# Performance work log

Hardware: AMD Instinct MI355X
Metric: run time of the kernel (lower is better)

## Reference

```python
import jax, jax.numpy as jnp
import numpy as np

N_EMBD = 1024
D_FF = 4096
N_EXPERTS = 8
TOP_K = 2


def setup_inputs() -> dict:
    key = jax.random.key(0)
    k1, k2, k3, k4 = jax.random.split(key, 4)
    x = jax.random.normal(k1, (1, 2048, N_EMBD), dtype=jnp.float32)
    mask = jnp.ones((2048, N_EXPERTS), dtype=jnp.float32)
    Wr = jax.random.normal(k2, (N_EMBD, N_EXPERTS), dtype=jnp.float32) * 0.02
    W1 = jax.random.normal(k3, (N_EXPERTS, N_EMBD, D_FF), dtype=jnp.float32) * 0.02
    W2 = jax.random.normal(k4, (N_EXPERTS, D_FF, N_EMBD), dtype=jnp.float32) * 0.02
    return {"x": x, "mask": mask, "Wr": Wr, "W1": W1, "W2": W2}


def reference(x, mask, Wr, W1, W2):
    T = x.shape[0] * x.shape[1]
    xs = x.reshape(T, N_EMBD)                      # [T, d]
    router_logits = (xs @ Wr) * mask               # [T, E], masked as in MaskedMoE
    all_probs = jax.nn.softmax(router_logits, axis=-1)  # softmax_topk order
    weights, selected = jax.lax.top_k(all_probs, TOP_K)  # [T, K]
    # combine[t, e] = sum of routing weights where token t selected expert e
    combine = jnp.zeros((T, N_EXPERTS), dtype=xs.dtype)
    combine = combine.at[jnp.arange(T)[:, None], selected].add(weights)
    results = jnp.zeros_like(xs)
    for e in range(N_EXPERTS):  # fixed small expert count
        h = jax.nn.gelu(xs @ W1[e])                # [T, d_ff]
        out = h @ W2[e]                            # [T, d]
        results = results + combine[:, e:e + 1] * out
    return results.reshape(x.shape)
```

## Files before the change

### kernel.cpp

```cpp
#include <hip/hip_runtime.h>
#include <hip/hip_bf16.h>


#define T_TOK 2048
#define D_EMB 1024
#define DFF   4096
#define NE    8

typedef _Float16 f16x8 __attribute__((ext_vector_type(8)));
typedef _Float16 f16x4 __attribute__((ext_vector_type(4)));
typedef float    f32x4 __attribute__((ext_vector_type(4)));

__device__ __forceinline__ float gelu_tanh(float x) {
    const float c = 0.7978845608028654f;
    float z = c * (x + 0.044715f * x * x * x);
    float u = __expf(2.0f * z);
    float th = (u - 1.0f) / (u + 1.0f);
    return 0.5f * x * (1.0f + th);
}

__device__ __forceinline__ void gll(const void* g, void* l) {
    __builtin_amdgcn_global_load_lds((__attribute__((address_space(1))) void*)g,
                                     (__attribute__((address_space(3))) void*)l,
                                     16, 0, 0);
}

__global__ void k_zero(int* counts) {
    if (threadIdx.x < NE) counts[threadIdx.x] = 0;
}

__global__ __launch_bounds__(256) void k_cvt_x(const float4* __restrict__ x4,
                                               _Float16* __restrict__ xh) {
    int i = blockIdx.x * 256 + threadIdx.x;
    float4 v = x4[i];
    f16x4 o;
    o[0] = (_Float16)v.x; o[1] = (_Float16)v.y;
    o[2] = (_Float16)v.z; o[3] = (_Float16)v.w;
    *(f16x4*)(xh + (size_t)i * 4) = o;
}

__global__ __launch_bounds__(256) void k_transpose(
    const float* __restrict__ src, _Float16* __restrict__ dst,
    int src_ld, int dst_ld) {
    __shared__ float tile[64][65];
    int e = blockIdx.z;
    const float* S = src + (size_t)e * 4194304;
    _Float16* D = dst + (size_t)e * 4194304;
    int t = threadIdx.x;
    int kb = blockIdx.y * 64;
    int nb = blockIdx.x * 64;
#pragma unroll
    for (int i = 0; i < 4; i++) {
        int r = (t >> 4) + i * 16;
        int c = (t & 15) * 4;
        float4 v = *(const float4*)(S + (size_t)(kb + r) * src_ld + nb + c);
        tile[r][c + 0] = v.x; tile[r][c + 1] = v.y;
        tile[r][c + 2] = v.z; tile[r][c + 3] = v.w;
    }
    __syncthreads();
#pragma unroll
    for (int j = 0; j < 2; j++) {
        int idx = j * 256 + t;
        int n = idx >> 3, kc = idx & 7;
        f16x8 o;
#pragma unroll
        for (int u = 0; u < 8; u++) o[u] = (_Float16)tile[kc * 8 + u][n];
        *(f16x8*)(D + (size_t)(nb + n) * dst_ld + kb + kc * 8) = o;
    }
}

__global__ __launch_bounds__(256) void k_router(
    const float* __restrict__ x, const float* __restrict__ mask,
    const float* __restrict__ Wr,
    int* __restrict__ counts, int* __restrict__ elist,
    int* __restrict__ tok_e, int* __restrict__ tok_p, float* __restrict__ tok_w) {
    int wave = threadIdx.x >> 6;
    int lane = threadIdx.x & 63;
    int t = blockIdx.x * 4 + wave;
    if (t >= T_TOK) return;

    float acc[NE];
#pragma unroll
    for (int e = 0; e < NE; e++) acc[e] = 0.f;
    const float* xr = x + (size_t)t * D_EMB;
    for (int c = 0; c < D_EMB / 64; c++) {
        int i = c * 64 + lane;
        float xv = xr[i];
        const float* wr = Wr + (size_t)i * NE;
#pragma unroll
        for (int e = 0; e < NE; e++) acc[e] += xv * wr[e];
    }
#pragma unroll
    for (int e = 0; e < NE; e++) {
#pragma unroll
        for (int off = 32; off > 0; off >>= 1)
            acc[e] += __shfl_xor(acc[e], off);
    }
    if (lane == 0) {
        float p[NE];
        float mx = -1e30f;
#pragma unroll
        for (int e = 0; e < NE; e++) {
            p[e] = acc[e] * mask[t * NE + e];
            mx = fmaxf(mx, p[e]);
        }
        float s = 0.f;
#pragma unroll
        for (int e = 0; e < NE; e++) { p[e] = expf(p[e] - mx); s += p[e]; }
#pragma unroll
        for (int e = 0; e < NE; e++) p[e] /= s;
        int e0 = 0; float b0 = p[0];
#pragma unroll
        for (int e = 1; e < NE; e++) if (p[e] > b0) { b0 = p[e]; e0 = e; }
        int e1 = -1; float b1 = -1.f;
#pragma unroll
        for (int e = 0; e < NE; e++) if (e != e0 && p[e] > b1) { b1 = p[e]; e1 = e; }

        int pos0 = atomicAdd(&counts[e0], 1);
        elist[e0 * T_TOK + pos0] = t;
        tok_e[t * 2 + 0] = e0; tok_p[t * 2 + 0] = pos0; tok_w[t * 2 + 0] = b0;
        int pos1 = atomicAdd(&counts[e1], 1);
        elist[e1 * T_TOK + pos1] = t;
        tok_e[t * 2 + 1] = e1; tok_p[t * 2 + 1] = pos1; tok_w[t * 2 + 1] = b1;
    }
}

__global__ void k_prefix(const int* __restrict__ counts, int* __restrict__ base) {
    if (threadIdx.x == 0) {
        int s = 0;
        for (int e = 0; e < NE; e++) { base[e] = s; s += counts[e]; }
        base[NE] = s;
    }
}

__global__ __launch_bounds__(256) void k_gemm1(
    const _Float16* __restrict__ xh, const _Float16* __restrict__ BT,
    const int* __restrict__ counts, const int* __restrict__ base,
    const int* __restrict__ elist, _Float16* __restrict__ H) {
    int e = blockIdx.z;
    int cnt = counts[e];
    int p0 = blockIdx.y * 128;
    if (p0 >= cnt) return;
    int n0 = blockIdx.x * 128;
    const _Float16* B = BT + (size_t)e * 4194304;

    __shared__ _Float16 As[128 * 32];
    __shared__ _Float16 Bs[128 * 32];
    __shared__ int ttok[128];

    int tid = threadIdx.x;
    if (tid < 128) ttok[tid] = elist[e * T_TOK + min(p0 + tid, cnt - 1)];
    __syncthreads();

    int w = tid >> 6, lane = tid & 63;
    int c0 = tid, c1 = tid + 256;
    const _Float16* pA0 = xh + (size_t)ttok[c0 >> 2] * D_EMB + (c0 & 3) * 8;
    const _Float16* pA1 = xh + (size_t)ttok[c1 >> 2] * D_EMB + (c1 & 3) * 8;
    const _Float16* pB0 = B + (size_t)(n0 + (c0 >> 2)) * 1024 + (c0 & 3) * 8;
    const _Float16* pB1 = B + (size_t)(n0 + (c1 >> 2)) * 1024 + (c1 & 3) * 8;
    _Float16* ldsA0 = As + (w * 64) * 8;
    _Float16* ldsA1 = As + (256 + w * 64) * 8;
    _Float16* ldsB0 = Bs + (w * 64) * 8;
    _Float16* ldsB1 = Bs + (256 + w * 64) * 8;

    int wm = w >> 1, wn = w & 1;
    int lhi = lane >> 4, llo = lane & 15;
    const _Float16* arp = As + ((wm * 64 + llo) * 32 + lhi * 8);
    const _Float16* brp = Bs + ((wn * 64 + llo) * 32 + lhi * 8);

    f32x4 acc[4][4] = {};
    for (int k0 = 0; k0 < D_EMB; k0 += 32) {
        __syncthreads();
        gll(pA0, ldsA0); gll(pA1, ldsA1);
        gll(pB0, ldsB0); gll(pB1, ldsB1);
        pA0 += 32; pA1 += 32; pB0 += 32; pB1 += 32;
        __syncthreads();
        f16x8 a[4], b[4];
#pragma unroll
        for (int i = 0; i < 4; i++) {
            a[i] = *(const f16x8*)(arp + i * 512);
            b[i] = *(const f16x8*)(brp + i * 512);
        }
#pragma unroll
        for (int mt = 0; mt < 4; mt++)
#pragma unroll
            for (int nt = 0; nt < 4; nt++)
                acc[mt][nt] = __builtin_amdgcn_mfma_f32_16x16x32_f16(a[mt], b[nt], acc[mt][nt], 0, 0, 0);
    }

    int rowbase = base[e];
#pragma unroll
    for (int mt = 0; mt < 4; mt++) {
#pragma unroll
        for (int i = 0; i < 4; i++) {
            int p = p0 + wm * 64 + mt * 16 + lhi * 4 + i;
            if (p < cnt) {
                size_t rowoff = (size_t)(rowbase + p) * DFF + n0 + wn * 64 + llo;
#pragma unroll
                for (int nt = 0; nt < 4; nt++)
                    H[rowoff + nt * 16] = (_Float16)gelu_tanh(acc[mt][nt][i]);
            }
        }
    }
}

__global__ __launch_bounds__(256) void k_gemm2(
    const _Float16* __restrict__ H, const _Float16* __restrict__ BT,
    const int* __restrict__ counts, const int* __restrict__ base,
    float* __restrict__ O, int kh) {
    int e = blockIdx.z;
    int cnt = counts[e];
    int p0 = blockIdx.y * 128;
    if (p0 >= cnt) return;
    int n0 = blockIdx.x * 128;
    const _Float16* B = BT + (size_t)e * 4194304;
    int rowbase = base[e];

    __shared__ _Float16 As[128 * 32];
    __shared__ _Float16 Bs[128 * 32];

    int tid = threadIdx.x;
    int w = tid >> 6, lane = tid & 63;
    int c0 = tid, c1 = tid + 256;
    int r0 = rowbase + min(p0 + (c0 >> 2), cnt - 1);
    int r1 = rowbase + min(p0 + (c1 >> 2), cnt - 1);
    const _Float16* pA0 = H + (size_t)r0 * DFF + kh + (c0 & 3) * 8;
    const _Float16* pA1 = H + (size_t)r1 * DFF + kh + (c1 & 3) * 8;
    const _Float16* pB0 = B + (size_t)(n0 + (c0 >> 2)) * 4096 + kh + (c0 & 3) * 8;
    const _Float16* pB1 = B + (size_t)(n0 + (c1 >> 2)) * 4096 + kh + (c1 & 3) * 8;
    _Float16* ldsA0 = As + (w * 64) * 8;
    _Float16* ldsA1 = As + (256 + w * 64) * 8;
    _Float16* ldsB0 = Bs + (w * 64) * 8;
    _Float16* ldsB1 = Bs + (256 + w * 64) * 8;

    int wm = w >> 1, wn = w & 1;
    int lhi = lane >> 4, llo = lane & 15;
    const _Float16* arp = As + ((wm * 64 + llo) * 32 + lhi * 8);
    const _Float16* brp = Bs + ((wn * 64 + llo) * 32 + lhi * 8);

    f32x4 acc[4][4] = {};
    for (int k0 = 0; k0 < 2048; k0 += 32) {
        __syncthreads();
        gll(pA0, ldsA0); gll(pA1, ldsA1);
        gll(pB0, ldsB0); gll(pB1, ldsB1);
        pA0 += 32; pA1 += 32; pB0 += 32; pB1 += 32;
        __syncthreads();
        f16x8 a[4], b[4];
#pragma unroll
        for (int i = 0; i < 4; i++) {
            a[i] = *(const f16x8*)(arp + i * 512);
            b[i] = *(const f16x8*)(brp + i * 512);
        }
#pragma unroll
        for (int mt = 0; mt < 4; mt++)
#pragma unroll
            for (int nt = 0; nt < 4; nt++)
                acc[mt][nt] = __builtin_amdgcn_mfma_f32_16x16x32_f16(a[mt], b[nt], acc[mt][nt], 0, 0, 0);
    }

#pragma unroll
    for (int mt = 0; mt < 4; mt++) {
#pragma unroll
        for (int i = 0; i < 4; i++) {
            int p = p0 + wm * 64 + mt * 16 + lhi * 4 + i;
            if (p < cnt) {
                size_t o = (size_t)(rowbase + p) * D_EMB + n0 + wn * 64 + llo;
#pragma unroll
                for (int nt = 0; nt < 4; nt++)
                    O[o + nt * 16] = acc[mt][nt][i];
            }
        }
    }
}

__global__ __launch_bounds__(256) void k_final(
    const float* __restrict__ O0, const float* __restrict__ O1,
    const int* __restrict__ base,
    const int* __restrict__ tok_e, const int* __restrict__ tok_p,
    const float* __restrict__ tok_w, float* __restrict__ out) {
    int t = blockIdx.x;
    int r0 = base[tok_e[t * 2 + 0]] + tok_p[t * 2 + 0];
    int r1 = base[tok_e[t * 2 + 1]] + tok_p[t * 2 + 1];
    float w0 = tok_w[t * 2 + 0], w1 = tok_w[t * 2 + 1];
    int i = threadIdx.x * 4;
    float4 a0 = *(const float4*)(O0 + (size_t)r0 * D_EMB + i);
    float4 b0 = *(const float4*)(O1 + (size_t)r0 * D_EMB + i);
    float4 a1 = *(const float4*)(O0 + (size_t)r1 * D_EMB + i);
    float4 b1 = *(const float4*)(O1 + (size_t)r1 * D_EMB + i);
    float4 o;
    o.x = w0 * (a0.x + b0.x) + w1 * (a1.x + b1.x);
    o.y = w0 * (a0.y + b0.y) + w1 * (a1.y + b1.y);
    o.z = w0 * (a0.z + b0.z) + w1 * (a1.z + b1.z);
    o.w = w0 * (a0.w + b0.w) + w1 * (a1.w + b1.w);
    *(float4*)(out + (size_t)t * D_EMB + i) = o;
}

extern "C" void kernel_launch(void* const* d_in, const int* in_sizes, int n_in,
                              void* d_out, int out_size, void* d_ws, size_t ws_size,
                              hipStream_t stream) {
    const float* x    = (const float*)d_in[0];
    const float* mask = (const float*)d_in[1];
    const float* Wr   = (const float*)d_in[2];
    const float* W1   = (const float*)d_in[3];
    const float* W2   = (const float*)d_in[4];
    float* out = (float*)d_out;

    char* ws = (char*)d_ws;
    const size_t MB = 1024 * 1024;
    int*      counts = (int*)(ws + 0);
    int*      base   = (int*)(ws + 256);
    int*      elist  = (int*)(ws + 1024);
    int*      tok_e  = (int*)(ws + 1024 + 65536);
    int*      tok_p  = (int*)(ws + 1024 + 65536 + 16384);
    float*    tok_w  = (float*)(ws + 1024 + 65536 + 32768);
    _Float16* xh     = (_Float16*)(ws + 1 * MB);
    _Float16* W1T    = (_Float16*)(ws + 8 * MB);
    _Float16* W2T    = (_Float16*)(ws + 72 * MB);
    _Float16* H      = (_Float16*)(ws + 136 * MB);
    float*    O0     = (float*)(ws + 168 * MB);
    float*    O1     = (float*)(ws + 184 * MB);

    k_zero<<<1, 64, 0, stream>>>(counts);
    k_router<<<T_TOK / 4, 256, 0, stream>>>(x, mask, Wr, counts, elist, tok_e, tok_p, tok_w);
    k_prefix<<<1, 64, 0, stream>>>(counts, base);
    k_cvt_x<<<T_TOK * D_EMB / 4 / 256, 256, 0, stream>>>((const float4*)x, xh);
    k_transpose<<<dim3(64, 16, NE), 256, 0, stream>>>(W1, W1T, DFF, 1024);
    k_transpose<<<dim3(16, 64, NE), 256, 0, stream>>>(W2, W2T, D_EMB, 4096);

    k_gemm1<<<dim3(32, 16, NE), 256, 0, stream>>>(xh, W1T, counts, base, elist, H);
    k_gemm2<<<dim3(8, 16, NE), 256, 0, stream>>>(H, W2T, counts, base, O0, 0);
    k_gemm2<<<dim3(8, 16, NE), 256, 0, stream>>>(H, W2T, counts, base, O1, 2048);
    k_final<<<T_TOK, 256, 0, stream>>>(O0, O1, base, tok_e, tok_p, tok_w, out);
}
```

Measured before the change: 543.3 us.

## Fuse prep kernels, widen GEMM K-tile with swizzled LDS, split-K by four

```diff
diff --git a/kernel.cpp b/kernel.cpp
--- a/kernel.cpp
+++ b/kernel.cpp
@@ -8,15 +8,13 @@
 #define NE    8
 
 typedef _Float16 f16x8 __attribute__((ext_vector_type(8)));
-typedef _Float16 f16x4 __attribute__((ext_vector_type(4)));
 typedef float    f32x4 __attribute__((ext_vector_type(4)));
 
 __device__ __forceinline__ float gelu_tanh(float x) {
     const float c = 0.7978845608028654f;
     float z = c * (x + 0.044715f * x * x * x);
     float u = __expf(2.0f * z);
-    float th = (u - 1.0f) / (u + 1.0f);
-    return 0.5f * x * (1.0f + th);
+    return 0.5f * x * (1.0f + (u - 1.0f) / (u + 1.0f));
 }
 
 __device__ __forceinline__ void gll(const void* g, void* l) {
@@ -29,26 +27,79 @@
     if (threadIdx.x < NE) counts[threadIdx.x] = 0;
 }
 
-__global__ __launch_bounds__(256) void k_cvt_x(const float4* __restrict__ x4,
-                                               _Float16* __restrict__ xh) {
-    int i = blockIdx.x * 256 + threadIdx.x;
-    float4 v = x4[i];
-    f16x4 o;
-    o[0] = (_Float16)v.x; o[1] = (_Float16)v.y;
-    o[2] = (_Float16)v.z; o[3] = (_Float16)v.w;
-    *(f16x4*)(xh + (size_t)i * 4) = o;
+__global__ __launch_bounds__(256) void k_router(
+    const float* __restrict__ x, const float* __restrict__ mask,
+    const float* __restrict__ Wr, _Float16* __restrict__ xh,
+    int* __restrict__ counts, int* __restrict__ elist,
+    int* __restrict__ tok_e, int* __restrict__ tok_p, float* __restrict__ tok_w) {
+    int wave = threadIdx.x >> 6;
+    int lane = threadIdx.x & 63;
+    int t = blockIdx.x * 4 + wave;
+    if (t >= T_TOK) return;
+
+    float acc[NE];
+#pragma unroll
+    for (int e = 0; e < NE; e++) acc[e] = 0.f;
+    const float* xr = x + (size_t)t * D_EMB;
+    for (int c = 0; c < D_EMB / 64; c++) {
+        int i = c * 64 + lane;
+        float xv = xr[i];
+        xh[(size_t)t * D_EMB + i] = (_Float16)xv;
+        const float* wr = Wr + (size_t)i * NE;
+#pragma unroll
+        for (int e = 0; e < NE; e++) acc[e] += xv * wr[e];
+    }
+#pragma unroll
+    for (int e = 0; e < NE; e++) {
+#pragma unroll
+        for (int off = 32; off > 0; off >>= 1)
+            acc[e] += __shfl_xor(acc[e], off);
+    }
+    if (lane == 0) {
+        float p[NE];
+        float mx = -1e30f;
+#pragma unroll
+        for (int e = 0; e < NE; e++) {
+            p[e] = acc[e] * mask[t * NE + e];
+            mx = fmaxf(mx, p[e]);
+        }
+        float s = 0.f;
+#pragma unroll
+        for (int e = 0; e < NE; e++) { p[e] = expf(p[e] - mx); s += p[e]; }
+#pragma unroll
+        for (int e = 0; e < NE; e++) p[e] /= s;
+        int e0 = 0; float b0 = p[0];
+#pragma unroll
+        for (int e = 1; e < NE; e++) if (p[e] > b0) { b0 = p[e]; e0 = e; }
+        int e1 = -1; float b1 = -1.f;
+#pragma unroll
+        for (int e = 0; e < NE; e++) if (e != e0 && p[e] > b1) { b1 = p[e]; e1 = e; }
+
+        int pos0 = atomicAdd(&counts[e0], 1);
+        elist[e0 * T_TOK + pos0] = t;
+        tok_e[t * 2 + 0] = e0; tok_p[t * 2 + 0] = pos0; tok_w[t * 2 + 0] = b0;
+        int pos1 = atomicAdd(&counts[e1], 1);
+        elist[e1 * T_TOK + pos1] = t;
+        tok_e[t * 2 + 1] = e1; tok_p[t * 2 + 1] = pos1; tok_w[t * 2 + 1] = b1;
+    }
 }
 
 __global__ __launch_bounds__(256) void k_transpose(
-    const float* __restrict__ src, _Float16* __restrict__ dst,
-    int src_ld, int dst_ld) {
+    const float* __restrict__ W1, const float* __restrict__ W2,
+    _Float16* __restrict__ W1T, _Float16* __restrict__ W2T) {
     __shared__ float tile[64][65];
-    int e = blockIdx.z;
-    const float* S = src + (size_t)e * 4194304;
-    _Float16* D = dst + (size_t)e * 4194304;
+    int bz = blockIdx.z;
+    int e = bz & 7;
+    bool isW2 = bz >= 8;
+    const float* S = (isW2 ? W2 : W1) + (size_t)e * 4194304;
+    _Float16* D = (isW2 ? W2T : W1T) + (size_t)e * 4194304;
+    int src_ld = isW2 ? 1024 : 4096;
+    int dst_ld = isW2 ? 4096 : 1024;
+    int bx = blockIdx.x;
+    int nb, kb;
+    if (isW2) { nb = (bx & 15) * 64; kb = (bx >> 4) * 64; }
+    else      { nb = (bx & 63) * 64; kb = (bx >> 6) * 64; }
     int t = threadIdx.x;
-    int kb = blockIdx.y * 64;
-    int nb = blockIdx.x * 64;
 #pragma unroll
     for (int i = 0; i < 4; i++) {
         int r = (t >> 4) + i * 16;
@@ -69,83 +120,22 @@
     }
 }
 
-__global__ __launch_bounds__(256) void k_router(
-    const float* __restrict__ x, const float* __restrict__ mask,
-    const float* __restrict__ Wr,
-    int* __restrict__ counts, int* __restrict__ elist,
-    int* __restrict__ tok_e, int* __restrict__ tok_p, float* __restrict__ tok_w) {
-    int wave = threadIdx.x >> 6;
-    int lane = threadIdx.x & 63;
-    int t = blockIdx.x * 4 + wave;
-    if (t >= T_TOK) return;
-
-    float acc[NE];
-#pragma unroll
-    for (int e = 0; e < NE; e++) acc[e] = 0.f;
-    const float* xr = x + (size_t)t * D_EMB;
-    for (int c = 0; c < D_EMB / 64; c++) {
-        int i = c * 64 + lane;
-        float xv = xr[i];
-        const float* wr = Wr + (size_t)i * NE;
-#pragma unroll
-        for (int e = 0; e < NE; e++) acc[e] += xv * wr[e];
-    }
-#pragma unroll
-    for (int e = 0; e < NE; e++) {
-#pragma unroll
-        for (int off = 32; off > 0; off >>= 1)
-            acc[e] += __shfl_xor(acc[e], off);
-    }
-    if (lane == 0) {
-        float p[NE];
-        float mx = -1e30f;
-#pragma unroll
-        for (int e = 0; e < NE; e++) {
-            p[e] = acc[e] * mask[t * NE + e];
-            mx = fmaxf(mx, p[e]);
-        }
-        float s = 0.f;
-#pragma unroll
-        for (int e = 0; e < NE; e++) { p[e] = expf(p[e] - mx); s += p[e]; }
-#pragma unroll
-        for (int e = 0; e < NE; e++) p[e] /= s;
-        int e0 = 0; float b0 = p[0];
-#pragma unroll
-        for (int e = 1; e < NE; e++) if (p[e] > b0) { b0 = p[e]; e0 = e; }
-        int e1 = -1; float b1 = -1.f;
-#pragma unroll
-        for (int e = 0; e < NE; e++) if (e != e0 && p[e] > b1) { b1 = p[e]; e1 = e; }
-
-        int pos0 = atomicAdd(&counts[e0], 1);
-        elist[e0 * T_TOK + pos0] = t;
-        tok_e[t * 2 + 0] = e0; tok_p[t * 2 + 0] = pos0; tok_w[t * 2 + 0] = b0;
-        int pos1 = atomicAdd(&counts[e1], 1);
-        elist[e1 * T_TOK + pos1] = t;
-        tok_e[t * 2 + 1] = e1; tok_p[t * 2 + 1] = pos1; tok_w[t * 2 + 1] = b1;
-    }
-}
-
-__global__ void k_prefix(const int* __restrict__ counts, int* __restrict__ base) {
-    if (threadIdx.x == 0) {
-        int s = 0;
-        for (int e = 0; e < NE; e++) { base[e] = s; s += counts[e]; }
-        base[NE] = s;
-    }
-}
 
 __global__ __launch_bounds__(256) void k_gemm1(
     const _Float16* __restrict__ xh, const _Float16* __restrict__ BT,
-    const int* __restrict__ counts, const int* __restrict__ base,
-    const int* __restrict__ elist, _Float16* __restrict__ H) {
+    const int* __restrict__ counts, const int* __restrict__ elist,
+    _Float16* __restrict__ H) {
     int e = blockIdx.z;
     int cnt = counts[e];
     int p0 = blockIdx.y * 128;
     if (p0 >= cnt) return;
+    int rowbase = 0;
+    for (int i = 0; i < NE; i++) rowbase += (i < e) ? counts[i] : 0;
     int n0 = blockIdx.x * 128;
     const _Float16* B = BT + (size_t)e * 4194304;
 
-    __shared__ _Float16 As[128 * 32];
-    __shared__ _Float16 Bs[128 * 32];
+    __shared__ _Float16 As[128 * 64];
+    __shared__ _Float16 Bs[128 * 64];
     __shared__ int ttok[128];
 
     int tid = threadIdx.x;
@@ -153,42 +143,61 @@
     __syncthreads();
 
     int w = tid >> 6, lane = tid & 63;
-    int c0 = tid, c1 = tid + 256;
-    const _Float16* pA0 = xh + (size_t)ttok[c0 >> 2] * D_EMB + (c0 & 3) * 8;
-    const _Float16* pA1 = xh + (size_t)ttok[c1 >> 2] * D_EMB + (c1 & 3) * 8;
-    const _Float16* pB0 = B + (size_t)(n0 + (c0 >> 2)) * 1024 + (c0 & 3) * 8;
-    const _Float16* pB1 = B + (size_t)(n0 + (c1 >> 2)) * 1024 + (c1 & 3) * 8;
-    _Float16* ldsA0 = As + (w * 64) * 8;
-    _Float16* ldsA1 = As + (256 + w * 64) * 8;
-    _Float16* ldsB0 = Bs + (w * 64) * 8;
-    _Float16* ldsB1 = Bs + (256 + w * 64) * 8;
+    int rq = tid >> 3;
+    int cch = (tid & 7) ^ ((tid >> 3) & 7);
+    const _Float16* pA[4];
+    const _Float16* pB[4];
+    _Float16* lA[4];
+    _Float16* lB[4];
+#pragma unroll
+    for (int q = 0; q < 4; q++) {
+        int row = q * 32 + rq;
+        pA[q] = xh + (size_t)ttok[row] * D_EMB + cch * 8;
+        pB[q] = B + (size_t)(n0 + row) * 1024 + cch * 8;
+        lA[q] = As + (q * 256 + w * 64) * 8;
+        lB[q] = Bs + (q * 256 + w * 64) * 8;
+    }
 
     int wm = w >> 1, wn = w & 1;
     int lhi = lane >> 4, llo = lane & 15;
-    const _Float16* arp = As + ((wm * 64 + llo) * 32 + lhi * 8);
-    const _Float16* brp = Bs + ((wn * 64 + llo) * 32 + lhi * 8);
+    int m7 = llo & 7;
+    int kc0 = lhi ^ m7, kc1 = kc0 ^ 4;
+    const _Float16* arp0 = As + (wm * 64 + llo) * 64 + kc0 * 8;
+    const _Float16* arp1 = As + (wm * 64 + llo) * 64 + kc1 * 8;
+    const _Float16* brp0 = Bs + (wn * 64 + llo) * 64 + kc0 * 8;
+    const _Float16* brp1 = Bs + (wn * 64 + llo) * 64 + kc1 * 8;
 
     f32x4 acc[4][4] = {};
-    for (int k0 = 0; k0 < D_EMB; k0 += 32) {
+    for (int it = 0; it < 16; ++it) {
         __syncthreads();
-        gll(pA0, ldsA0); gll(pA1, ldsA1);
-        gll(pB0, ldsB0); gll(pB1, ldsB1);
-        pA0 += 32; pA1 += 32; pB0 += 32; pB1 += 32;
+#pragma unroll
+        for (int q = 0; q < 4; q++) { gll(pA[q], lA[q]); gll(pB[q], lB[q]); }
+#pragma unroll
+        for (int q = 0; q < 4; q++) { pA[q] += 64; pB[q] += 64; }
         __syncthreads();
         f16x8 a[4], b[4];
 #pragma unroll
         for (int i = 0; i < 4; i++) {
-            a[i] = *(const f16x8*)(arp + i * 512);
-            b[i] = *(const f16x8*)(brp + i * 512);
+            a[i] = *(const f16x8*)(arp0 + i * 1024);
+            b[i] = *(const f16x8*)(brp0 + i * 1024);
         }
 #pragma unroll
         for (int mt = 0; mt < 4; mt++)
 #pragma unroll
             for (int nt = 0; nt < 4; nt++)
                 acc[mt][nt] = __builtin_amdgcn_mfma_f32_16x16x32_f16(a[mt], b[nt], acc[mt][nt], 0, 0, 0);
-    }
-
-    int rowbase = base[e];
+#pragma unroll
+        for (int i = 0; i < 4; i++) {
+            a[i] = *(const f16x8*)(arp1 + i * 1024);
+            b[i] = *(const f16x8*)(brp1 + i * 1024);
+        }
+#pragma unroll
+        for (int mt = 0; mt < 4; mt++)
+#pragma unroll
+            for (int nt = 0; nt < 4; nt++)
+                acc[mt][nt] = __builtin_amdgcn_mfma_f32_16x16x32_f16(a[mt], b[nt], acc[mt][nt], 0, 0, 0);
+    }
+
 #pragma unroll
     for (int mt = 0; mt < 4; mt++) {
 #pragma unroll
@@ -206,50 +215,72 @@
 
 __global__ __launch_bounds__(256) void k_gemm2(
     const _Float16* __restrict__ H, const _Float16* __restrict__ BT,
-    const int* __restrict__ counts, const int* __restrict__ base,
-    float* __restrict__ O, int kh) {
-    int e = blockIdx.z;
+    const int* __restrict__ counts, float* __restrict__ Obase) {
+    int bz = blockIdx.z;
+    int e = bz & 7, sp = bz >> 3;
     int cnt = counts[e];
     int p0 = blockIdx.y * 128;
     if (p0 >= cnt) return;
+    int rowbase = 0;
+    for (int i = 0; i < NE; i++) rowbase += (i < e) ? counts[i] : 0;
     int n0 = blockIdx.x * 128;
+    int kh = sp * 1024;
     const _Float16* B = BT + (size_t)e * 4194304;
-    int rowbase = base[e];
-
-    __shared__ _Float16 As[128 * 32];
-    __shared__ _Float16 Bs[128 * 32];
+    float* O = Obase + (size_t)sp * 4194304;
+
+    __shared__ _Float16 As[128 * 64];
+    __shared__ _Float16 Bs[128 * 64];
 
     int tid = threadIdx.x;
     int w = tid >> 6, lane = tid & 63;
-    int c0 = tid, c1 = tid + 256;
-    int r0 = rowbase + min(p0 + (c0 >> 2), cnt - 1);
-    int r1 = rowbase + min(p0 + (c1 >> 2), cnt - 1);
-    const _Float16* pA0 = H + (size_t)r0 * DFF + kh + (c0 & 3) * 8;
-    const _Float16* pA1 = H + (size_t)r1 * DFF + kh + (c1 & 3) * 8;
-    const _Float16* pB0 = B + (size_t)(n0 + (c0 >> 2)) * 4096 + kh + (c0 & 3) * 8;
-    const _Float16* pB1 = B + (size_t)(n0 + (c1 >> 2)) * 4096 + kh + (c1 & 3) * 8;
-    _Float16* ldsA0 = As + (w * 64) * 8;
-    _Float16* ldsA1 = As + (256 + w * 64) * 8;
-    _Float16* ldsB0 = Bs + (w * 64) * 8;
-    _Float16* ldsB1 = Bs + (256 + w * 64) * 8;
+    int rq = tid >> 3;
+    int cch = (tid & 7) ^ ((tid >> 3) & 7);
+    const _Float16* pA[4];
+    const _Float16* pB[4];
+    _Float16* lA[4];
+    _Float16* lB[4];
+#pragma unroll
+    for (int q = 0; q < 4; q++) {
+        int row = q * 32 + rq;
+        int r = rowbase + min(p0 + row, cnt - 1);
+        pA[q] = H + (size_t)r * DFF + kh + cch * 8;
+        pB[q] = B + (size_t)(n0 + row) * 4096 + kh + cch * 8;
+        lA[q] = As + (q * 256 + w * 64) * 8;
+        lB[q] = Bs + (q * 256 + w * 64) * 8;
+    }
 
     int wm = w >> 1, wn = w & 1;
     int lhi = lane >> 4, llo = lane & 15;
-    const _Float16* arp = As + ((wm * 64 + llo) * 32 + lhi * 8);
-    const _Float16* brp = Bs + ((wn * 64 + llo) * 32 + lhi * 8);
+    int m7 = llo & 7;
+    int kc0 = lhi ^ m7, kc1 = kc0 ^ 4;
+    const _Float16* arp0 = As + (wm * 64 + llo) * 64 + kc0 * 8;
+    const _Float16* arp1 = As + (wm * 64 + llo) * 64 + kc1 * 8;
+    const _Float16* brp0 = Bs + (wn * 64 + llo) * 64 + kc0 * 8;
+    const _Float16* brp1 = Bs + (wn * 64 + llo) * 64 + kc1 * 8;
 
     f32x4 acc[4][4] = {};
-    for (int k0 = 0; k0 < 2048; k0 += 32) {
+    for (int it = 0; it < 16; ++it) {
         __syncthreads();
-        gll(pA0, ldsA0); gll(pA1, ldsA1);
-        gll(pB0, ldsB0); gll(pB1, ldsB1);
-        pA0 += 32; pA1 += 32; pB0 += 32; pB1 += 32;
+#pragma unroll
+        for (int q = 0; q < 4; q++) { gll(pA[q], lA[q]); gll(pB[q], lB[q]); }
+#pragma unroll
+        for (int q = 0; q < 4; q++) { pA[q] += 64; pB[q] += 64; }
         __syncthreads();
         f16x8 a[4], b[4];
 #pragma unroll
         for (int i = 0; i < 4; i++) {
-            a[i] = *(const f16x8*)(arp + i * 512);
-            b[i] = *(const f16x8*)(brp + i * 512);
+            a[i] = *(const f16x8*)(arp0 + i * 1024);
+            b[i] = *(const f16x8*)(brp0 + i * 1024);
+        }
+#pragma unroll
+        for (int mt = 0; mt < 4; mt++)
+#pragma unroll
+            for (int nt = 0; nt < 4; nt++)
+                acc[mt][nt] = __builtin_amdgcn_mfma_f32_16x16x32_f16(a[mt], b[nt], acc[mt][nt], 0, 0, 0);
+#pragma unroll
+        for (int i = 0; i < 4; i++) {
+            a[i] = *(const f16x8*)(arp1 + i * 1024);
+            b[i] = *(const f16x8*)(brp1 + i * 1024);
         }
 #pragma unroll
         for (int mt = 0; mt < 4; mt++)
@@ -274,24 +305,34 @@
 }
 
 __global__ __launch_bounds__(256) void k_final(
-    const float* __restrict__ O0, const float* __restrict__ O1,
-    const int* __restrict__ base,
+    const float* __restrict__ Obase, const int* __restrict__ counts,
     const int* __restrict__ tok_e, const int* __restrict__ tok_p,
     const float* __restrict__ tok_w, float* __restrict__ out) {
+    __shared__ int sb[NE];
     int t = blockIdx.x;
-    int r0 = base[tok_e[t * 2 + 0]] + tok_p[t * 2 + 0];
-    int r1 = base[tok_e[t * 2 + 1]] + tok_p[t * 2 + 1];
+    if (threadIdx.x == 0) {
+        int s = 0;
+        for (int e = 0; e < NE; e++) { sb[e] = s; s += counts[e]; }
+    }
+    __syncthreads();
+    int r0 = sb[tok_e[t * 2 + 0]] + tok_p[t * 2 + 0];
+    int r1 = sb[tok_e[t * 2 + 1]] + tok_p[t * 2 + 1];
     float w0 = tok_w[t * 2 + 0], w1 = tok_w[t * 2 + 1];
     int i = threadIdx.x * 4;
-    float4 a0 = *(const float4*)(O0 + (size_t)r0 * D_EMB + i);
-    float4 b0 = *(const float4*)(O1 + (size_t)r0 * D_EMB + i);
-    float4 a1 = *(const float4*)(O0 + (size_t)r1 * D_EMB + i);
-    float4 b1 = *(const float4*)(O1 + (size_t)r1 * D_EMB + i);
+    float4 s0 = {0, 0, 0, 0}, s1 = {0, 0, 0, 0};
+#pragma unroll
+    for (int sp = 0; sp < 4; sp++) {
+        const float* O = Obase + (size_t)sp * 4194304;
+        float4 a = *(const float4*)(O + (size_t)r0 * D_EMB + i);
+        float4 b = *(const float4*)(O + (size_t)r1 * D_EMB + i);
+        s0.x += a.x; s0.y += a.y; s0.z += a.z; s0.w += a.w;
+        s1.x += b.x; s1.y += b.y; s1.z += b.z; s1.w += b.w;
+    }
     float4 o;
-    o.x = w0 * (a0.x + b0.x) + w1 * (a1.x + b1.x);
-    o.y = w0 * (a0.y + b0.y) + w1 * (a1.y + b1.y);
-    o.z = w0 * (a0.z + b0.z) + w1 * (a1.z + b1.z);
-    o.w = w0 * (a0.w + b0.w) + w1 * (a1.w + b1.w);
+    o.x = w0 * s0.x + w1 * s1.x;
+    o.y = w0 * s0.y + w1 * s1.y;
+    o.z = w0 * s0.z + w1 * s1.z;
+    o.w = w0 * s0.w + w1 * s1.w;
     *(float4*)(out + (size_t)t * D_EMB + i) = o;
 }
 
@@ -308,7 +349,6 @@
     char* ws = (char*)d_ws;
     const size_t MB = 1024 * 1024;
     int*      counts = (int*)(ws + 0);
-    int*      base   = (int*)(ws + 256);
     int*      elist  = (int*)(ws + 1024);
     int*      tok_e  = (int*)(ws + 1024 + 65536);
     int*      tok_p  = (int*)(ws + 1024 + 65536 + 16384);
@@ -317,18 +357,12 @@
     _Float16* W1T    = (_Float16*)(ws + 8 * MB);
     _Float16* W2T    = (_Float16*)(ws + 72 * MB);
     _Float16* H      = (_Float16*)(ws + 136 * MB);
-    float*    O0     = (float*)(ws + 168 * MB);
-    float*    O1     = (float*)(ws + 184 * MB);
+    float*    Obuf   = (float*)(ws + 168 * MB);
 
     k_zero<<<1, 64, 0, stream>>>(counts);
-    k_router<<<T_TOK / 4, 256, 0, stream>>>(x, mask, Wr, counts, elist, tok_e, tok_p, tok_w);
-    k_prefix<<<1, 64, 0, stream>>>(counts, base);
-    k_cvt_x<<<T_TOK * D_EMB / 4 / 256, 256, 0, stream>>>((const float4*)x, xh);
-    k_transpose<<<dim3(64, 16, NE), 256, 0, stream>>>(W1, W1T, DFF, 1024);
-    k_transpose<<<dim3(16, 64, NE), 256, 0, stream>>>(W2, W2T, D_EMB, 4096);
-
-    k_gemm1<<<dim3(32, 16, NE), 256, 0, stream>>>(xh, W1T, counts, base, elist, H);
-    k_gemm2<<<dim3(8, 16, NE), 256, 0, stream>>>(H, W2T, counts, base, O0, 0);
-    k_gemm2<<<dim3(8, 16, NE), 256, 0, stream>>>(H, W2T, counts, base, O1, 2048);
-    k_final<<<T_TOK, 256, 0, stream>>>(O0, O1, base, tok_e, tok_p, tok_w, out);
-}
+    k_router<<<T_TOK / 4, 256, 0, stream>>>(x, mask, Wr, xh, counts, elist, tok_e, tok_p, tok_w);
+    k_transpose<<<dim3(1024, 1, 16), 256, 0, stream>>>(W1, W2, W1T, W2T);
+    k_gemm1<<<dim3(32, 16, NE), 256, 0, stream>>>(xh, W1T, counts, elist, H);
+    k_gemm2<<<dim3(8, 16, 32), 256, 0, stream>>>(H, W2T, counts, Obuf);
+    k_final<<<T_TOK, 256, 0, stream>>>(Obuf, counts, tok_e, tok_p, tok_w, out);
+}
```

Result: faster. 506.8 us (-6.7%).
